# Optimization experiments

Measured on AMD Instinct MI355X. Metric: run time of the kernel, lower is better.

## Reference

```python
import jax, jax.numpy as jnp
import numpy as np

EPS = 1e-5

def _layernorm_per_head(x, gamma, beta):
    # x: [b, h, L, d]; gamma, beta: [h, d] (distinct LayerNorm per head)
    mu = jnp.mean(x, axis=-1, keepdims=True)
    var = jnp.var(x, axis=-1, keepdims=True)
    xhat = (x - mu) * jax.lax.rsqrt(var + EPS)
    return xhat * gamma[None, :, None, :] + beta[None, :, None, :]

def setup_inputs() -> dict:
    key = jax.random.key(0)
    ks = jax.random.split(key, 10)
    b, nx, ny, nt = 2, 32, 32, 32
    cin, d, h = 128, 128, 8
    hd = h * d
    s_in = 1.0 / np.sqrt(cin)
    s_hd = 1.0 / np.sqrt(hd)
    return {
        "v": jax.random.normal(ks[0], (b, nx, ny, nt, cin), dtype=jnp.float32),
        "Wq_w": jax.random.normal(ks[1], (cin, hd), dtype=jnp.float32) * s_in,
        "Wq_b": jnp.zeros((hd,), dtype=jnp.float32),
        "Wk_w": jax.random.normal(ks[2], (cin, hd), dtype=jnp.float32) * s_in,
        "Wk_b": jnp.zeros((hd,), dtype=jnp.float32),
        "Wv_w": jax.random.normal(ks[3], (cin, hd), dtype=jnp.float32) * s_in,
        "Wv_b": jnp.zeros((hd,), dtype=jnp.float32),
        "Wo_w": jax.random.normal(ks[4], (hd, d), dtype=jnp.float32) * s_hd,
        "Wo_b": jnp.zeros((d,), dtype=jnp.float32),
        "lnk_g": jnp.ones((h, d), dtype=jnp.float32),
        "lnk_b": jnp.zeros((h, d), dtype=jnp.float32),
        "lnv_g": jnp.ones((h, d), dtype=jnp.float32),
        "lnv_b": jnp.zeros((h, d), dtype=jnp.float32),
    }

def reference(v, Wq_w, Wq_b, Wk_w, Wk_b, Wv_w, Wv_b, Wo_w, Wo_b,
              lnk_g, lnk_b, lnv_g, lnv_b):
    b, nx, ny, nt, cin = v.shape
    h, d = lnk_g.shape
    L = nx * ny * nt
    n = nx * ny  # NOTE: original divides by nx*ny only (not nt)
    x = v.reshape(b, L, cin)
    # projections -> [b, h, L, d]
    def proj(W, bias):
        y = x @ W + bias  # [b, L, h*d]
        return y.reshape(b, L, h, d).transpose(0, 2, 1, 3)
    Q = proj(Wq_w, Wq_b)
    K = proj(Wk_w, Wk_b)
    V = proj(Wv_w, Wv_b)
    K = _layernorm_per_head(K, lnk_g, lnk_b)
    V = _layernorm_per_head(V, lnv_g, lnv_b)
    # linear (Galerkin) attention: K^T V then Q (K^T V)
    attn_map = jnp.einsum('bhmd,bhmc->bhdc', K, V)      # [b, h, d, d]
    attn_out = jnp.einsum('bhld,bhdc->bhlc', Q, attn_map)  # [b, h, L, d]
    attn_out = attn_out.transpose(0, 2, 1, 3).reshape(b, L, h * d)
    out = (attn_out @ Wo_w + Wo_b) / n
    return out.reshape(b, nx, ny, nt, d)
```

## Files before the change

kernel.cpp:

```cpp
#include <hip/hip_runtime.h>
#include <stdint.h>

typedef unsigned short u16;
typedef unsigned int u32;
typedef __attribute__((ext_vector_type(8))) short s16x8;
typedef __attribute__((ext_vector_type(8))) __bf16 bf16x8;
typedef __attribute__((ext_vector_type(4))) float f32x4;
typedef __attribute__((ext_vector_type(2))) float f32x2;
typedef __attribute__((ext_vector_type(4))) u16 u16x4;

#define L_TOT 32768
#define NCH 16

__device__ __forceinline__ u32 f2bf(float f){
  u32 u = __builtin_bit_cast(u32, f);
  return (u + 0x7FFFu + ((u >> 16) & 1u)) >> 16;
}

__device__ __forceinline__ f32x4 mfma16(s16x8 a, s16x8 b, f32x4 c){
  return __builtin_amdgcn_mfma_f32_16x16x32_bf16(
      __builtin_bit_cast(bf16x8, a), __builtin_bit_cast(bf16x8, b), c, 0, 0, 0);
}

__device__ __forceinline__ void gload16(const void* g, void* l){
  __builtin_amdgcn_global_load_lds(
      (const __attribute__((address_space(1))) void*)g,
      (__attribute__((address_space(3))) void*)l, 16, 0, 0);
}

__device__ __forceinline__ u32 cvtpk(float lo, float hi){
  u32 r;
  asm("v_cvt_pk_bf16_f32 %0, %1, %2" : "=v"(r) : "v"(lo), "v"(hi));
  return r;
}

__device__ __forceinline__ float dpp_reduce16(float x){
  float y;
  asm("v_add_f32_dpp %0, %1, %1 row_ror:8 row_mask:0xf bank_mask:0xf"
      : "=&v"(y) : "v"(x));
  asm("v_add_f32_dpp %0, %1, %1 row_ror:4 row_mask:0xf bank_mask:0xf"
      : "=&v"(x) : "v"(y));
  asm("v_add_f32_dpp %0, %1, %1 quad_perm:[2,3,0,1] row_mask:0xf bank_mask:0xf"
      : "=&v"(y) : "v"(x));
  asm("v_add_f32_dpp %0, %1, %1 quad_perm:[1,0,3,2] row_mask:0xf bank_mask:0xf"
      : "=&v"(x) : "v"(y));
  return x;
}

__global__ void kprep(const float* __restrict__ v, const float* __restrict__ Wk,
                      const float* __restrict__ Wv, u16* __restrict__ X,
                      u16* __restrict__ WkF, u16* __restrict__ WvF){
  int tid = blockIdx.x * blockDim.x + threadIdx.x;
  int stride = gridDim.x * blockDim.x;
  for (int i = tid; i < 2097152; i += stride){
    float4 f = *((const float4*)v + i);
    u16x4 o; o.x = (u16)f2bf(f.x); o.y = (u16)f2bf(f.y); o.z = (u16)f2bf(f.z); o.w = (u16)f2bf(f.w);
    *((u16x4*)X + i) = o;
  }
  for (int i = tid; i < 131072; i += stride){
    int e = i & 7, ln = (i >> 3) & 63, ks = (i >> 9) & 3, nt = (i >> 11) & 7, h = i >> 14;
    int c = ks * 32 + (ln >> 4) * 8 + e;
    int n = nt * 16 + (ln & 15);
    int src = c * 1024 + h * 128 + n;
    WkF[i] = (u16)f2bf(Wk[src]);
    WvF[i] = (u16)f2bf(Wv[src]);
  }
}

__global__ __launch_bounds__(512, 2) void kattn(
    const u16* __restrict__ X, const u16* __restrict__ WkF, const u16* __restrict__ WvF,
    const float* __restrict__ bk, const float* __restrict__ bv,
    float* __restrict__ G, float* __restrict__ KBar, float* __restrict__ VBar)
{
  extern __shared__ char smem[];
  char* sWK = smem;
  char* sWV = smem + 32768;
  char* sKF = smem + 65536;
  char* sVF = smem + 98304;

  const int tid = threadIdx.x;
  const int wid = tid >> 6, lane = tid & 63, g = lane >> 4, l15 = lane & 15;
  const int bh = blockIdx.x >> 4, grp = blockIdx.x & 15;
  const int b = bh >> 3, h = bh & 7;
  const bool isK = (wid < 4);
  const int w4 = wid & 3;

  {
    const char* gwk = (const char*)(WkF + h * 16384);
    const char* gwv = (const char*)(WvF + h * 16384);
    #pragma unroll
    for (int c = 0; c < 4; ++c){
      u32 o = (u32)(c * 8192 + tid * 16);
      gload16(gwk + o, sWK + o);
      gload16(gwv + o, sWV + o);
    }
  }
  const float* bias = isK ? bk : bv;
  float br[8];
  #pragma unroll
  for (int nt = 0; nt < 8; ++nt) br[nt] = bias[h * 128 + nt * 16 + l15];

  asm volatile("s_waitcnt vmcnt(0)" ::: "memory");
  __builtin_amdgcn_s_barrier();

  const char* sW = isK ? sWK : sWV;
  char* sT = isK ? sKF : sVF;
  const u16* Xb = X + (size_t)b * (L_TOT * 128);

  const u32 wread = (u32)(lane * 16);
  char* stbase = sT + (((g >> 1) * 16 + l15) * 16 + (g & 1) * 8 + w4 * 1024);
  const char* kfbase = sKF + lane * 16;
  const char* vfbase = sVF + lane * 16;
  const char* xlane = (const char*)Xb + (w4 * 32 + l15) * 256 + g * 16;

  f32x4 am[4][2];
  #pragma unroll
  for (int t = 0; t < 4; ++t)
    #pragma unroll
    for (int u2 = 0; u2 < 2; ++u2) am[t][u2] = f32x4{0.f, 0.f, 0.f, 0.f};
  f32x2 kb2[8];
  #pragma unroll
  for (int nt = 0; nt < 8; ++nt) kb2[nt] = f32x2{0.f, 0.f};

#define PREF(dst, it) { \
  const char* p_ = xlane + (size_t)((grp * NCH + (it)) * 128) * 256; \
  _Pragma("unroll") for (int mt_ = 0; mt_ < 2; ++mt_) \
  _Pragma("unroll") for (int ks_ = 0; ks_ < 4; ++ks_) \
    dst[mt_][ks_] = *(const s16x8*)(p_ + mt_ * 4096 + ks_ * 64); }

#define BODY(F) { \
    f32x4 acc[2][8]; \
    _Pragma("unroll") for (int mt = 0; mt < 2; ++mt) \
      _Pragma("unroll") for (int nt = 0; nt < 8; ++nt) acc[mt][nt] = f32x4{0.f,0.f,0.f,0.f}; \
    _Pragma("unroll") for (int ks = 0; ks < 4; ++ks){ \
      _Pragma("unroll") for (int nt = 0; nt < 8; ++nt){ \
        s16x8 wf = *(const s16x8*)(sW + wread + (nt * 4 + ks) * 1024); \
        acc[0][nt] = mfma16(F[0][ks], wf, acc[0][nt]); \
        acc[1][nt] = mfma16(F[1][ks], wf, acc[1][nt]); \
      } \
    } \
    _Pragma("unroll") for (int mt = 0; mt < 2; ++mt){ \
      f32x4 sum = {0.f,0.f,0.f,0.f}, sq = {0.f,0.f,0.f,0.f}; \
      _Pragma("unroll") for (int nt = 0; nt < 8; ++nt){ \
        f32x4 t = acc[mt][nt] + f32x4{br[nt], br[nt], br[nt], br[nt]}; \
        acc[mt][nt] = t; sum += t; sq += t * t; \
      } \
      f32x4 s4, ns4; \
      _Pragma("unroll") for (int j = 0; j < 4; ++j){ \
        float ssum = dpp_reduce16(sum[j]); \
        float ssq  = dpp_reduce16(sq[j]); \
        float mean = ssum * 0.0078125f; \
        float var  = ssq * 0.0078125f - mean * mean; \
        float rstd = rsqrtf(var + 1e-5f); \
        s4[j] = rstd; ns4[j] = -mean * rstd; \
      } \
      _Pragma("unroll") for (int nt = 0; nt < 8; ++nt){ \
        f32x4 t = acc[mt][nt] * s4 + ns4; \
        kb2[nt] += f32x2{t.x, t.y} + f32x2{t.z, t.w}; \
        uint2 w_; w_.x = cvtpk(t.x, t.y); w_.y = cvtpk(t.z, t.w); \
        *(uint2*)(stbase + nt * 4096 + mt * 512) = w_; \
      } \
    } \
    asm volatile("s_waitcnt lgkmcnt(0)" ::: "memory"); \
    __builtin_amdgcn_s_barrier(); \
    { \
      const int dkt = (wid >> 2) * 4; \
      _Pragma("unroll") for (int kk = 0; kk < 4; ++kk){ \
        s16x8 a2[4], b2[2]; \
        _Pragma("unroll") for (int t = 0; t < 4; ++t) \
          a2[t] = *(const s16x8*)(kfbase + (dkt + t) * 4096 + kk * 1024); \
        _Pragma("unroll") for (int u2 = 0; u2 < 2; ++u2) \
          b2[u2] = *(const s16x8*)(vfbase + (w4 * 2 + u2) * 4096 + kk * 1024); \
        _Pragma("unroll") for (int t = 0; t < 4; ++t) \
          _Pragma("unroll") for (int u2 = 0; u2 < 2; ++u2) \
            am[t][u2] = mfma16(a2[t], b2[u2], am[t][u2]); \
      } \
    } \
    __builtin_amdgcn_s_barrier(); \
  }

  s16x8 af[2][4], afn[2][4];
  PREF(af, 0);
  #pragma unroll 1
  for (int it2 = 0; it2 < NCH; it2 += 2){
    PREF(afn, it2 + 1);
    BODY(af);
    PREF(af, (it2 + 2 < NCH) ? it2 + 2 : 0);
    BODY(afn);
  }
#undef BODY
#undef PREF

  float* Gbh = G + (size_t)bh * 16384;
  #pragma unroll
  for (int t = 0; t < 4; ++t)
    #pragma unroll
    for (int u2 = 0; u2 < 2; ++u2)
      #pragma unroll
      for (int j = 0; j < 4; ++j){
        int dk = (wid >> 2) * 64 + t * 16 + g * 4 + j;
        int dv = w4 * 32 + u2 * 16 + l15;
        atomicAdd(Gbh + dk * 128 + dv, am[t][u2][j]);
      }
  float* dstB = (isK ? KBar : VBar) + bh * 128;
  #pragma unroll
  for (int nt = 0; nt < 8; ++nt){
    float kb = kb2[nt].x + kb2[nt].y;
    kb += __shfl_xor(kb, 16);
    kb += __shfl_xor(kb, 32);
    if (g == 0) atomicAdd(dstB + nt * 16 + l15, kb);
  }
}

__global__ __launch_bounds__(256) void kfold(
    const float* __restrict__ G, const float* __restrict__ KBar, const float* __restrict__ VBar,
    const float* __restrict__ gk, const float* __restrict__ bbk,
    const float* __restrict__ gv, const float* __restrict__ bbv,
    const float* __restrict__ Wo, const float* __restrict__ Wq,
    const float* __restrict__ Wq_b, const float* __restrict__ Wo_b,
    float* __restrict__ W4, float* __restrict__ c4)
{
  extern __shared__ float fsm[];
  float* sA = fsm;
  float* sS = fsm + 128 * 129;
  int blk = blockIdx.x;
  int bh = blk >> 2, eq = blk & 3;
  int b = bh >> 3, hs = bh & 7;
  int tid = threadIdx.x;

  const float* gkh = gk + hs * 128; const float* bkh = bbk + hs * 128;
  const float* gvh = gv + hs * 128; const float* bvh = bbv + hs * 128;
  const float* kbh = KBar + bh * 128; const float* vbh = VBar + bh * 128;

  for (int idx = tid; idx < 16384; idx += 256){
    int r = idx >> 7, c = idx & 127;
    float gg = G[(size_t)bh * 16384 + idx];
    float am = gkh[r] * (gvh[c] * gg + kbh[r] * bvh[c])
             + bkh[r] * (gvh[c] * vbh[c] + 32768.f * bvh[c]);
    sA[r * 129 + c] = am;
  }
  for (int idx = tid; idx < 4096; idx += 256){
    int r = idx >> 5, c = idx & 31;
    sS[r * 33 + c] = Wo[(size_t)hs * 16384 + r * 128 + eq * 32 + c];
  }
  __syncthreads();

  int r0 = (tid >> 4) * 8, e0 = (tid & 15) * 2;
  float t8[8][2] = {};
  for (int c = 0; c < 128; ++c){
    float wv0 = sS[c * 33 + e0], wv1 = sS[c * 33 + e0 + 1];
    #pragma unroll
    for (int i = 0; i < 8; ++i){
      float a = sA[(r0 + i) * 129 + c];
      t8[i][0] += a * wv0; t8[i][1] += a * wv1;
    }
  }
  __syncthreads();
  #pragma unroll
  for (int i = 0; i < 8; ++i){
    sS[(r0 + i) * 33 + e0]     = t8[i][0];
    sS[(r0 + i) * 33 + e0 + 1] = t8[i][1];
  }
  for (int idx = tid; idx < 16384; idx += 256){
    int r = idx >> 7, c = idx & 127;
    sA[r * 129 + c] = Wq[(size_t)r * 1024 + hs * 128 + c];
  }
  __syncthreads();

  float a8[8][2] = {};
  for (int d = 0; d < 128; ++d){
    float t0 = sS[d * 33 + e0], t1 = sS[d * 33 + e0 + 1];
    #pragma unroll
    for (int i = 0; i < 8; ++i){
      float w = sA[(r0 + i) * 129 + d];
      a8[i][0] += w * t0; a8[i][1] += w * t1;
    }
  }
  const float inv_n = 0.0009765625f;
  #pragma unroll
  for (int i = 0; i < 8; ++i){
    atomicAdd(W4 + (size_t)b * 16384 + (r0 + i) * 128 + eq * 32 + e0,     a8[i][0] * inv_n);
    atomicAdd(W4 + (size_t)b * 16384 + (r0 + i) * 128 + eq * 32 + e0 + 1, a8[i][1] * inv_n);
  }
  if (tid < 32){
    float s = 0.f;
    for (int d = 0; d < 128; ++d) s += Wq_b[hs * 128 + d] * sS[d * 33 + tid];
    if (hs == 0) s += Wo_b[eq * 32 + tid];
    atomicAdd(c4 + b * 128 + eq * 32 + tid, s * inv_n);
  }
}

__global__ void kfold3(const float* __restrict__ W4, u16* __restrict__ W4T){
  int i = blockIdx.x * 256 + threadIdx.x;
  if (i >= 32768) return;
  int b = i >> 14, o = i & 16383;
  int e = o & 7, ln = (o >> 3) & 63, ks = (o >> 9) & 3, nt = (o >> 11) & 7;
  int c = ks * 32 + (ln >> 4) * 8 + e;
  int n = nt * 16 + (ln & 15);
  W4T[i] = (u16)f2bf(W4[(size_t)b * 16384 + c * 128 + n]);
}

__global__ __launch_bounds__(256, 4) void kout(
    const u16* __restrict__ X, const u16* __restrict__ W4T,
    const float* __restrict__ c4, float* __restrict__ out)
{
  __shared__ char sW[32768];
  const int tid = threadIdx.x, wid = tid >> 6, lane = tid & 63, g = lane >> 4, l15 = lane & 15;
  const int blk = blockIdx.x, b = blk >> 8, ch = blk & 255;
  {
    const char* gw = (const char*)(W4T + (size_t)b * 16384);
    #pragma unroll
    for (int c = 0; c < 8; ++c){
      u32 o = (u32)(c * 4096 + tid * 16);
      gload16(gw + o, sW + o);
    }
  }
  const char* xr = (const char*)(X + ((size_t)b * L_TOT + ch * 128 + wid * 32 + l15) * 128) + g * 16;
  s16x8 af[2][4];
  #pragma unroll
  for (int mt = 0; mt < 2; ++mt)
    #pragma unroll
    for (int ks = 0; ks < 4; ++ks)
      af[mt][ks] = *(const s16x8*)(xr + mt * 4096 + ks * 64);
  asm volatile("s_waitcnt vmcnt(0)" ::: "memory");
  __builtin_amdgcn_s_barrier();

  f32x4 acc[2][8];
  #pragma unroll
  for (int mt = 0; mt < 2; ++mt)
    #pragma unroll
    for (int nt = 0; nt < 8; ++nt) acc[mt][nt] = f32x4{0.f, 0.f, 0.f, 0.f};

  const u32 wread = (u32)(lane * 16);
  #pragma unroll
  for (int ks = 0; ks < 4; ++ks)
    #pragma unroll
    for (int nt = 0; nt < 8; ++nt){
      s16x8 wf = *(const s16x8*)(sW + wread + (nt * 4 + ks) * 1024);
      acc[0][nt] = mfma16(af[0][ks], wf, acc[0][nt]);
      acc[1][nt] = mfma16(af[1][ks], wf, acc[1][nt]);
    }
  float* ob = out + ((size_t)b * L_TOT + ch * 128 + wid * 32) * 128;
  #pragma unroll
  for (int nt = 0; nt < 8; ++nt){
    float c4v = c4[b * 128 + nt * 16 + l15];
    #pragma unroll
    for (int mt = 0; mt < 2; ++mt)
      #pragma unroll
      for (int j = 0; j < 4; ++j)
        ob[(mt * 16 + g * 4 + j) * 128 + nt * 16 + l15] = acc[mt][nt][j] + c4v;
  }
}

extern "C" void kernel_launch(void* const* d_in, const int* in_sizes, int n_in,
                              void* d_out, int out_size, void* d_ws, size_t ws_size,
                              hipStream_t stream){
  const float* v    = (const float*)d_in[0];
  const float* Wq_w = (const float*)d_in[1];
  const float* Wq_b = (const float*)d_in[2];
  const float* Wk_w = (const float*)d_in[3];
  const float* Wk_b = (const float*)d_in[4];
  const float* Wv_w = (const float*)d_in[5];
  const float* Wv_b = (const float*)d_in[6];
  const float* Wo_w = (const float*)d_in[7];
  const float* Wo_b = (const float*)d_in[8];
  const float* lnk_g = (const float*)d_in[9];
  const float* lnk_b = (const float*)d_in[10];
  const float* lnv_g = (const float*)d_in[11];
  const float* lnv_b = (const float*)d_in[12];

  char* ws = (char*)d_ws;
  u16*   X    = (u16*)  (ws);
  u16*   WkF  = (u16*)  (ws + 16777216);
  u16*   WvF  = (u16*)  (ws + 17039360);
  float* G    = (float*)(ws + 17301504);
  float* KBar = (float*)(ws + 18350080);
  float* VBar = (float*)(ws + 18358272);
  float* W4   = (float*)(ws + 18366464);
  float* c4   = (float*)(ws + 18497536);
  u16*   W4T  = (u16*)  (ws + 18498560);

  hipMemsetAsync(ws + 17301504, 0, 1197056, stream);

  hipLaunchKernelGGL(kprep, dim3(2048), dim3(256), 0, stream, v, Wk_w, Wv_w, X, WkF, WvF);

  (void)hipFuncSetAttribute((const void*)kattn,
                            hipFuncAttributeMaxDynamicSharedMemorySize, 131072);
  hipLaunchKernelGGL(kattn, dim3(256), dim3(512), 131072, stream,
                     X, WkF, WvF, Wk_b, Wv_b, G, KBar, VBar);

  (void)hipFuncSetAttribute((const void*)kfold,
                            hipFuncAttributeMaxDynamicSharedMemorySize, 83968);
  hipLaunchKernelGGL(kfold, dim3(64), dim3(256), 83968, stream,
                     G, KBar, VBar, lnk_g, lnk_b, lnv_g, lnv_b,
                     Wo_w, Wq_w, Wq_b, Wo_b, W4, c4);
  hipLaunchKernelGGL(kfold3, dim3(128), dim3(256), 0, stream, W4, W4T);

  hipLaunchKernelGGL(kout, dim3(512), dim3(256), 0, stream, X, W4T, c4, (float*)d_out);
}
```

Measured before the change: 144.0 us.

## Software-pipeline attention projection with K^T V accumulation and drop kfold3 kernel

Restructures the kattn main loop so the K/V projection MFMAs for the next chunk are interleaved with the K^T V accumulation MFMAs of the previous chunk. This removes one barrier-separated phase per chunk, and s_setprio raises priority over the MFMA region. Normalized K/V fragments are now built in registers with permlane swaps and stored as full 16-byte LDS writes instead of scattered 8-byte ones. kfold writes W4 directly in the MFMA fragment layout and kout converts it to bf16 on load, which removes the kfold3 launch. The price is more register pressure from the extra live fragments and accumulators, plus more complex loop peeling.

```diff
diff --git a/kernel.cpp b/kernel.cpp
--- a/kernel.cpp
+++ b/kernel.cpp
@@ -6,7 +6,7 @@
 typedef __attribute__((ext_vector_type(8))) short s16x8;
 typedef __attribute__((ext_vector_type(8))) __bf16 bf16x8;
 typedef __attribute__((ext_vector_type(4))) float f32x4;
-typedef __attribute__((ext_vector_type(2))) float f32x2;
+typedef __attribute__((ext_vector_type(4))) u32 u32x4;
 typedef __attribute__((ext_vector_type(4))) u16 u16x4;
 
 #define L_TOT 32768
@@ -47,6 +47,43 @@
   return x;
 }
 
+__device__ __forceinline__ s16x8 build_frag(f32x4 t0, f32x4 t1){
+  u32 p0 = cvtpk(t0.x, t0.y);
+  u32 p1 = cvtpk(t0.z, t0.w);
+  u32 p2 = cvtpk(t1.x, t1.y);
+  u32 p3 = cvtpk(t1.z, t1.w);
+  asm("v_permlane32_swap_b32 %0, %1" : "+v"(p0), "+v"(p2));
+  asm("v_permlane16_swap_b32 %0, %1" : "+v"(p0), "+v"(p2));
+  asm("v_permlane32_swap_b32 %0, %1" : "+v"(p1), "+v"(p3));
+  asm("v_permlane16_swap_b32 %0, %1" : "+v"(p1), "+v"(p3));
+  u32x4 r; r.x = p0; r.y = p1; r.z = p2; r.w = p3;
+  return __builtin_bit_cast(s16x8, r);
+}
+
+__device__ __forceinline__ void ln_center(f32x4 (&acc)[2][8], const float (&br)[8]){
+  #pragma unroll
+  for (int mt = 0; mt < 2; ++mt){
+    f32x4 sum = {0.f,0.f,0.f,0.f}, sq = {0.f,0.f,0.f,0.f};
+    #pragma unroll
+    for (int nt = 0; nt < 8; ++nt){
+      f32x4 t = acc[mt][nt] + f32x4{br[nt], br[nt], br[nt], br[nt]};
+      acc[mt][nt] = t; sum += t; sq += t * t;
+    }
+    f32x4 s4, ns4;
+    #pragma unroll
+    for (int j = 0; j < 4; ++j){
+      float ss = dpp_reduce16(sum[j]);
+      float qq = dpp_reduce16(sq[j]);
+      float mean = ss * 0.0078125f;
+      float var  = qq * 0.0078125f - mean * mean;
+      float rstd = rsqrtf(var + 1e-5f);
+      s4[j] = rstd; ns4[j] = -mean * rstd;
+    }
+    #pragma unroll
+    for (int nt = 0; nt < 8; ++nt) acc[mt][nt] = acc[mt][nt] * s4 + ns4;
+  }
+}
+
 __global__ void kprep(const float* __restrict__ v, const float* __restrict__ Wk,
                       const float* __restrict__ Wv, u16* __restrict__ X,
                       u16* __restrict__ WkF, u16* __restrict__ WvF){
@@ -80,10 +117,11 @@
 
   const int tid = threadIdx.x;
   const int wid = tid >> 6, lane = tid & 63, g = lane >> 4, l15 = lane & 15;
-  const int bh = blockIdx.x >> 4, grp = blockIdx.x & 15;
+  const int bh = blockIdx.x >> 4, lgrp = blockIdx.x & 15;
   const int b = bh >> 3, h = bh & 7;
   const bool isK = (wid < 4);
   const int w4 = wid & 3;
+  const int dkt = (wid >> 2) * 4;
 
   {
     const char* gwk = (const char*)(WkF + h * 16384);
@@ -100,95 +138,113 @@
   #pragma unroll
   for (int nt = 0; nt < 8; ++nt) br[nt] = bias[h * 128 + nt * 16 + l15];
 
-  asm volatile("s_waitcnt vmcnt(0)" ::: "memory");
-  __builtin_amdgcn_s_barrier();
-
   const char* sW = isK ? sWK : sWV;
-  char* sT = isK ? sKF : sVF;
+  char* stf = (isK ? sKF : sVF) + w4 * 1024 + lane * 16;
+  const char* kfb = sKF + lane * 16;
+  const char* vfb = sVF + lane * 16;
   const u16* Xb = X + (size_t)b * (L_TOT * 128);
-
+  const char* xlane = (const char*)Xb
+      + ((size_t)(lgrp * (NCH * 128)) + w4 * 32 + l15) * 256 + g * 16;
   const u32 wread = (u32)(lane * 16);
-  char* stbase = sT + (((g >> 1) * 16 + l15) * 16 + (g & 1) * 8 + w4 * 1024);
-  const char* kfbase = sKF + lane * 16;
-  const char* vfbase = sVF + lane * 16;
-  const char* xlane = (const char*)Xb + (w4 * 32 + l15) * 256 + g * 16;
 
   f32x4 am[4][2];
   #pragma unroll
   for (int t = 0; t < 4; ++t)
     #pragma unroll
-    for (int u2 = 0; u2 < 2; ++u2) am[t][u2] = f32x4{0.f, 0.f, 0.f, 0.f};
-  f32x2 kb2[8];
-  #pragma unroll
-  for (int nt = 0; nt < 8; ++nt) kb2[nt] = f32x2{0.f, 0.f};
+    for (int u2 = 0; u2 < 2; ++u2) am[t][u2] = f32x4{0.f,0.f,0.f,0.f};
+  float kbv[8] = {0,0,0,0,0,0,0,0};
+  s16x8 afA[2][4], afB[2][4], cf[8];
 
 #define PREF(dst, it) { \
-  const char* p_ = xlane + (size_t)((grp * NCH + (it)) * 128) * 256; \
+  const char* p_ = xlane + (size_t)(it) * 32768; \
   _Pragma("unroll") for (int mt_ = 0; mt_ < 2; ++mt_) \
   _Pragma("unroll") for (int ks_ = 0; ks_ < 4; ++ks_) \
     dst[mt_][ks_] = *(const s16x8*)(p_ + mt_ * 4096 + ks_ * 64); }
 
-#define BODY(F) { \
+#define LNBUILD(ACC) { \
+    ln_center(ACC, br); \
+    _Pragma("unroll") for (int nt = 0; nt < 8; ++nt){ \
+      f32x4 s_ = ACC[0][nt] + ACC[1][nt]; \
+      kbv[nt] += (s_.x + s_.y) + (s_.z + s_.w); \
+      cf[nt] = build_frag(ACC[0][nt], ACC[1][nt]); \
+    } }
+
+#define STORECF() { \
+    _Pragma("unroll") for (int nt = 0; nt < 8; ++nt) \
+      *(s16x8*)(stf + nt * 4096) = cf[nt]; \
+    asm volatile("s_waitcnt lgkmcnt(0)" ::: "memory"); \
+    __builtin_amdgcn_sched_barrier(0); }
+
+#define BAR() { asm volatile("" ::: "memory"); \
+    __builtin_amdgcn_s_barrier(); \
+    asm volatile("" ::: "memory"); }
+
+#define SPAN(FCUR, FPRE, prefit, DO_NEXT) { \
     f32x4 acc[2][8]; \
-    _Pragma("unroll") for (int mt = 0; mt < 2; ++mt) \
-      _Pragma("unroll") for (int nt = 0; nt < 8; ++nt) acc[mt][nt] = f32x4{0.f,0.f,0.f,0.f}; \
-    _Pragma("unroll") for (int ks = 0; ks < 4; ++ks){ \
-      _Pragma("unroll") for (int nt = 0; nt < 8; ++nt){ \
-        s16x8 wf = *(const s16x8*)(sW + wread + (nt * 4 + ks) * 1024); \
-        acc[0][nt] = mfma16(F[0][ks], wf, acc[0][nt]); \
-        acc[1][nt] = mfma16(F[1][ks], wf, acc[1][nt]); \
+    if (DO_NEXT){ \
+      _Pragma("unroll") for (int mt = 0; mt < 2; ++mt) \
+        _Pragma("unroll") for (int nt = 0; nt < 8; ++nt) acc[mt][nt] = f32x4{0.f,0.f,0.f,0.f}; \
+    } \
+    __builtin_amdgcn_s_setprio(1); \
+    _Pragma("unroll") for (int ks2 = 0; ks2 < 4; ++ks2){ \
+      s16x8 a2[4], b2[2]; \
+      _Pragma("unroll") for (int t = 0; t < 4; ++t) \
+        a2[t] = *(const s16x8*)(kfb + (dkt + t) * 4096 + ks2 * 1024); \
+      _Pragma("unroll") for (int u2 = 0; u2 < 2; ++u2) \
+        b2[u2] = *(const s16x8*)(vfb + (w4 * 2 + u2) * 4096 + ks2 * 1024); \
+      if (DO_NEXT){ \
+        _Pragma("unroll") for (int nt = 0; nt < 8; ++nt){ \
+          s16x8 wf = *(const s16x8*)(sW + wread + (nt * 4 + ks2) * 1024); \
+          acc[0][nt] = mfma16(FCUR[0][ks2], wf, acc[0][nt]); \
+          acc[1][nt] = mfma16(FCUR[1][ks2], wf, acc[1][nt]); \
+        } \
       } \
+      _Pragma("unroll") for (int t = 0; t < 4; ++t) \
+        _Pragma("unroll") for (int u2 = 0; u2 < 2; ++u2) \
+          am[t][u2] = mfma16(a2[t], b2[u2], am[t][u2]); \
     } \
-    _Pragma("unroll") for (int mt = 0; mt < 2; ++mt){ \
-      f32x4 sum = {0.f,0.f,0.f,0.f}, sq = {0.f,0.f,0.f,0.f}; \
-      _Pragma("unroll") for (int nt = 0; nt < 8; ++nt){ \
-        f32x4 t = acc[mt][nt] + f32x4{br[nt], br[nt], br[nt], br[nt]}; \
-        acc[mt][nt] = t; sum += t; sq += t * t; \
-      } \
-      f32x4 s4, ns4; \
-      _Pragma("unroll") for (int j = 0; j < 4; ++j){ \
-        float ssum = dpp_reduce16(sum[j]); \
-        float ssq  = dpp_reduce16(sq[j]); \
-        float mean = ssum * 0.0078125f; \
-        float var  = ssq * 0.0078125f - mean * mean; \
-        float rstd = rsqrtf(var + 1e-5f); \
-        s4[j] = rstd; ns4[j] = -mean * rstd; \
-      } \
-      _Pragma("unroll") for (int nt = 0; nt < 8; ++nt){ \
-        f32x4 t = acc[mt][nt] * s4 + ns4; \
-        kb2[nt] += f32x2{t.x, t.y} + f32x2{t.z, t.w}; \
-        uint2 w_; w_.x = cvtpk(t.x, t.y); w_.y = cvtpk(t.z, t.w); \
-        *(uint2*)(stbase + nt * 4096 + mt * 512) = w_; \
-      } \
+    __builtin_amdgcn_s_setprio(0); \
+    if (DO_NEXT){ \
+      PREF(FPRE, prefit); \
+      LNBUILD(acc); \
     } \
-    asm volatile("s_waitcnt lgkmcnt(0)" ::: "memory"); \
-    __builtin_amdgcn_s_barrier(); \
-    { \
-      const int dkt = (wid >> 2) * 4; \
-      _Pragma("unroll") for (int kk = 0; kk < 4; ++kk){ \
-        s16x8 a2[4], b2[2]; \
-        _Pragma("unroll") for (int t = 0; t < 4; ++t) \
-          a2[t] = *(const s16x8*)(kfbase + (dkt + t) * 4096 + kk * 1024); \
-        _Pragma("unroll") for (int u2 = 0; u2 < 2; ++u2) \
-          b2[u2] = *(const s16x8*)(vfbase + (w4 * 2 + u2) * 4096 + kk * 1024); \
-        _Pragma("unroll") for (int t = 0; t < 4; ++t) \
-          _Pragma("unroll") for (int u2 = 0; u2 < 2; ++u2) \
-            am[t][u2] = mfma16(a2[t], b2[u2], am[t][u2]); \
-      } \
-    } \
-    __builtin_amdgcn_s_barrier(); \
-  }
-
-  s16x8 af[2][4], afn[2][4];
-  PREF(af, 0);
+    BAR(); \
+    if (DO_NEXT){ STORECF(); } \
+    BAR(); }
+
+  PREF(afA, 0);
+  PREF(afB, 1);
+  asm volatile("s_waitcnt vmcnt(0)" ::: "memory");
+  BAR();
+  {
+    f32x4 acc[2][8];
+    #pragma unroll
+    for (int mt = 0; mt < 2; ++mt)
+      #pragma unroll
+      for (int nt = 0; nt < 8; ++nt) acc[mt][nt] = f32x4{0.f,0.f,0.f,0.f};
+    #pragma unroll
+    for (int ks = 0; ks < 4; ++ks)
+      #pragma unroll
+      for (int nt = 0; nt < 8; ++nt){
+        s16x8 wf = *(const s16x8*)(sW + wread + (nt * 4 + ks) * 1024);
+        acc[0][nt] = mfma16(afA[0][ks], wf, acc[0][nt]);
+        acc[1][nt] = mfma16(afA[1][ks], wf, acc[1][nt]);
+      }
+    LNBUILD(acc);
+  }
+  STORECF();
+  BAR();
+
   #pragma unroll 1
-  for (int it2 = 0; it2 < NCH; it2 += 2){
-    PREF(afn, it2 + 1);
-    BODY(af);
-    PREF(af, (it2 + 2 < NCH) ? it2 + 2 : 0);
-    BODY(afn);
-  }
-#undef BODY
+  for (int i = 0; i < NCH; i += 2){
+    SPAN(afB, afA, (i + 2 < NCH) ? (i + 2) : 0, true);
+    if (i + 1 < NCH - 1){ SPAN(afA, afB, (i + 3 < NCH) ? (i + 3) : 0, true); }
+    else                { SPAN(afA, afB, 0, false); }
+  }
+#undef SPAN
+#undef BAR
+#undef STORECF
+#undef LNBUILD
 #undef PREF
 
   float* Gbh = G + (size_t)bh * 16384;
@@ -205,10 +261,9 @@
   float* dstB = (isK ? KBar : VBar) + bh * 128;
   #pragma unroll
   for (int nt = 0; nt < 8; ++nt){
-    float kb = kb2[nt].x + kb2[nt].y;
-    kb += __shfl_xor(kb, 16);
-    kb += __shfl_xor(kb, 32);
-    if (g == 0) atomicAdd(dstB + nt * 16 + l15, kb);
+    float s = kbv[nt];
+    s += __shfl_xor(s, 16); s += __shfl_xor(s, 32);
+    if (g == 0) atomicAdd(dstB + nt * 16 + l15, s);
   }
 }
 
@@ -218,7 +273,7 @@
     const float* __restrict__ gv, const float* __restrict__ bbv,
     const float* __restrict__ Wo, const float* __restrict__ Wq,
     const float* __restrict__ Wq_b, const float* __restrict__ Wo_b,
-    float* __restrict__ W4, float* __restrict__ c4)
+    float* __restrict__ W4F, float* __restrict__ c4)
 {
   extern __shared__ float fsm[];
   float* sA = fsm;
@@ -235,9 +290,9 @@
   for (int idx = tid; idx < 16384; idx += 256){
     int r = idx >> 7, c = idx & 127;
     float gg = G[(size_t)bh * 16384 + idx];
-    float am = gkh[r] * (gvh[c] * gg + kbh[r] * bvh[c])
-             + bkh[r] * (gvh[c] * vbh[c] + 32768.f * bvh[c]);
-    sA[r * 129 + c] = am;
+    float amv = gkh[r] * (gvh[c] * gg + kbh[r] * bvh[c])
+              + bkh[r] * (gvh[c] * vbh[c] + 32768.f * bvh[c]);
+    sA[r * 129 + c] = amv;
   }
   for (int idx = tid; idx < 4096; idx += 256){
     int r = idx >> 5, c = idx & 31;
@@ -278,10 +333,14 @@
   }
   const float inv_n = 0.0009765625f;
   #pragma unroll
-  for (int i = 0; i < 8; ++i){
-    atomicAdd(W4 + (size_t)b * 16384 + (r0 + i) * 128 + eq * 32 + e0,     a8[i][0] * inv_n);
-    atomicAdd(W4 + (size_t)b * 16384 + (r0 + i) * 128 + eq * 32 + e0 + 1, a8[i][1] * inv_n);
-  }
+  for (int i = 0; i < 8; ++i)
+    #pragma unroll
+    for (int j = 0; j < 2; ++j){
+      int cc = r0 + i, nn = eq * 32 + e0 + j;
+      int o = ((nn >> 4) * 4 + (cc >> 5)) * 512 + ((cc >> 3) & 3) * 128
+            + (nn & 15) * 8 + (cc & 7);
+      atomicAdd(W4F + (size_t)b * 16384 + o, a8[i][j] * inv_n);
+    }
   if (tid < 32){
     float s = 0.f;
     for (int d = 0; d < 128; ++d) s += Wq_b[hs * 128 + d] * sS[d * 33 + tid];
@@ -290,29 +349,21 @@
   }
 }
 
-__global__ void kfold3(const float* __restrict__ W4, u16* __restrict__ W4T){
-  int i = blockIdx.x * 256 + threadIdx.x;
-  if (i >= 32768) return;
-  int b = i >> 14, o = i & 16383;
-  int e = o & 7, ln = (o >> 3) & 63, ks = (o >> 9) & 3, nt = (o >> 11) & 7;
-  int c = ks * 32 + (ln >> 4) * 8 + e;
-  int n = nt * 16 + (ln & 15);
-  W4T[i] = (u16)f2bf(W4[(size_t)b * 16384 + c * 128 + n]);
-}
-
 __global__ __launch_bounds__(256, 4) void kout(
-    const u16* __restrict__ X, const u16* __restrict__ W4T,
+    const u16* __restrict__ X, const float* __restrict__ W4F,
     const float* __restrict__ c4, float* __restrict__ out)
 {
   __shared__ char sW[32768];
   const int tid = threadIdx.x, wid = tid >> 6, lane = tid & 63, g = lane >> 4, l15 = lane & 15;
   const int blk = blockIdx.x, b = blk >> 8, ch = blk & 255;
   {
-    const char* gw = (const char*)(W4T + (size_t)b * 16384);
-    #pragma unroll
-    for (int c = 0; c < 8; ++c){
-      u32 o = (u32)(c * 4096 + tid * 16);
-      gload16(gw + o, sW + o);
+    const float* w4b = W4F + (size_t)b * 16384;
+    #pragma unroll
+    for (int it2 = 0; it2 < 16; ++it2){
+      int idx = it2 * 1024 + tid * 4;
+      float4 f = *(const float4*)(w4b + idx);
+      uint2 w; w.x = cvtpk(f.x, f.y); w.y = cvtpk(f.z, f.w);
+      *(uint2*)(sW + idx * 2) = w;
     }
   }
   const char* xr = (const char*)(X + ((size_t)b * L_TOT + ch * 128 + wid * 32 + l15) * 128) + g * 16;
@@ -322,8 +373,7 @@
     #pragma unroll
     for (int ks = 0; ks < 4; ++ks)
       af[mt][ks] = *(const s16x8*)(xr + mt * 4096 + ks * 64);
-  asm volatile("s_waitcnt vmcnt(0)" ::: "memory");
-  __builtin_amdgcn_s_barrier();
+  __syncthreads();
 
   f32x4 acc[2][8];
   #pragma unroll
@@ -376,9 +426,8 @@
   float* G    = (float*)(ws + 17301504);
   float* KBar = (float*)(ws + 18350080);
   float* VBar = (float*)(ws + 18358272);
-  float* W4   = (float*)(ws + 18366464);
+  float* W4F  = (float*)(ws + 18366464);
   float* c4   = (float*)(ws + 18497536);
-  u16*   W4T  = (u16*)  (ws + 18498560);
 
   hipMemsetAsync(ws + 17301504, 0, 1197056, stream);
 
@@ -393,8 +442,7 @@
                             hipFuncAttributeMaxDynamicSharedMemorySize, 83968);
   hipLaunchKernelGGL(kfold, dim3(64), dim3(256), 83968, stream,
                      G, KBar, VBar, lnk_g, lnk_b, lnv_g, lnv_b,
-                     Wo_w, Wq_w, Wq_b, Wo_b, W4, c4);
-  hipLaunchKernelGGL(kfold3, dim3(128), dim3(256), 0, stream, W4, W4T);
-
-  hipLaunchKernelGGL(kout, dim3(512), dim3(256), 0, stream, X, W4T, c4, (float*)d_out);
-}
+                     Wo_w, Wq_w, Wq_b, Wo_b, W4F, c4);
+
+  hipLaunchKernelGGL(kout, dim3(512), dim3(256), 0, stream, X, W4F, c4, (float*)d_out);
+}
```

Measured after the change: 155.6 us. 1.08x slower.
